# Performance work log

Measured on AMD Instinct MI355X. Metric: run time of the kernel, lower is better.

The kernel has to match this reference:

```python
import jax, jax.numpy as jnp
import numpy as np

N, E = 50000, 800000
H, C_HID = 4, 64  # heads, hidden_units
C_IN, C_OUT = 256, 64
NEG_SLOPE = 0.2
EPS = 1e-16


def gat_conv(x, src, dst, W, att_src, att_dst, bias):
    """PyG GATConv with concat=False (mean over heads) + bias.
    x: [N, F_in], W: [F_in, H*C], att_*: [H, C], bias: [C]."""
    n = x.shape[0]
    h = (x @ W).reshape(n, H, -1)                     # [N, H, C]
    a_src = jnp.sum(h * att_src, axis=-1)             # [N, H]
    a_dst = jnp.sum(h * att_dst, axis=-1)             # [N, H]
    e = jax.nn.leaky_relu(a_src[src] + a_dst[dst], NEG_SLOPE)  # [E, H]
    # segment softmax grouped by destination node
    m = jax.ops.segment_max(e, dst, num_segments=n)   # [N, H]
    e = jnp.exp(e - m[dst])
    denom = jax.ops.segment_sum(e, dst, num_segments=n)
    alpha = e / (denom[dst] + EPS)                    # [E, H]
    msg = h[src] * alpha[:, :, None]                  # [E, H, C]
    out = jax.ops.segment_sum(msg, dst, num_segments=n)  # [N, H, C]
    return out.mean(axis=1) + bias                    # concat=False -> head mean


def setup_inputs() -> dict:
    key = jax.random.key(0)
    ks = jax.random.split(key, 16)
    inp = {
        "x": jax.random.normal(ks[0], (N, C_IN), dtype=jnp.float32),
        "edge_index": jax.random.randint(ks[1], (2, E), 0, N, dtype=jnp.int64),
    }
    dims = [(C_IN, C_HID), (C_HID, C_HID), (C_HID, C_OUT)]
    for i, (fi, fo) in enumerate(dims, start=1):
        inp[f"W{i}"] = jax.random.normal(ks[2 + 4 * (i - 1)], (fi, H * fo), dtype=jnp.float32) * (1.0 / np.sqrt(fi))
        inp[f"as{i}"] = jax.random.normal(ks[3 + 4 * (i - 1)], (H, fo), dtype=jnp.float32) * 0.1
        inp[f"ad{i}"] = jax.random.normal(ks[4 + 4 * (i - 1)], (H, fo), dtype=jnp.float32) * 0.1
        inp[f"b{i}"] = jnp.zeros((fo,), dtype=jnp.float32)
    return inp


def reference(x, edge_index, W1, as1, ad1, b1, W2, as2, ad2, b2, W3, as3, ad3, b3):
    n = x.shape[0]
    loop = jnp.arange(n, dtype=edge_index.dtype)
    src = jnp.concatenate([edge_index[0], loop])  # add_self_loops=True (PyG default)
    dst = jnp.concatenate([edge_index[1], loop])
    layers = [(W1, as1, ad1, b1), (W2, as2, ad2, b2), (W3, as3, ad3, b3)]
    for (W, a_s, a_d, b) in layers:
        x = gat_conv(x, src, dst, W, a_s, a_d, b)
        x = jax.nn.relu(x)  # dropout is identity at inference
    return jax.nn.log_softmax(x, axis=-1)
```

## Files before the change

kernel.cpp:

```cpp
#include <hip/hip_runtime.h>
#include <hip/hip_bf16.h>
#include <math.h>
#include <stdint.h>

#define HEADS 4
#define CH 64
#define HC 256
#define NEG 0.2f
#define EPSV 1e-16f
#define NEGBIG -3.0e38f

typedef __attribute__((ext_vector_type(8))) short short8;
typedef __attribute__((ext_vector_type(4))) float f32x4;
typedef _Float16 f16_t;
typedef __fp16 fp16x2 __attribute__((ext_vector_type(2)));

__device__ __forceinline__ float lrelu(float x) { return x > 0.f ? x : NEG * x; }

__device__ __forceinline__ unsigned short f2bf(float f) {
  __hip_bfloat16 b = __float2bfloat16(f);
  return *reinterpret_cast<unsigned short*>(&b);
}
__device__ __forceinline__ float bf2f(unsigned short u) {
  return __uint_as_float((unsigned)u << 16);
}
__device__ __forceinline__ unsigned int pkf16(float a, float b) {
  fp16x2 v = __builtin_amdgcn_cvt_pkrtz(a, b);
  return __builtin_bit_cast(unsigned int, v);
}
__device__ __forceinline__ float dot2acc(unsigned int a, unsigned int h, float acc) {
#if __has_builtin(__builtin_amdgcn_fdot2)
  return __builtin_amdgcn_fdot2(__builtin_bit_cast(fp16x2, a),
                                __builtin_bit_cast(fp16x2, h), acc, false);
#else
  fp16x2 av = __builtin_bit_cast(fp16x2, a);
  fp16x2 hv = __builtin_bit_cast(fp16x2, h);
  return acc + (float)av[0] * (float)hv[0] + (float)av[1] * (float)hv[1];
#endif
}

__global__ __launch_bounds__(256) void wprep_k(const float* __restrict__ W,
                                               unsigned short* __restrict__ Wt,
                                               int K) {
  int i = blockIdx.x * 256 + threadIdx.x;
  if (i >= K * 256) return;
  int k = i >> 8, n = i & 255;
  Wt[(size_t)n * K + k] = f2bf(W[i]);
}

__global__ __launch_bounds__(256) void mfma_gat_k(const float* __restrict__ Af,
                                                  const unsigned short* __restrict__ Ab,
                                                  const unsigned short* __restrict__ Wt,
                                                  const float* __restrict__ att_s,
                                                  const float* __restrict__ att_d,
                                                  unsigned short* __restrict__ ht16,
                                                  float* __restrict__ a_src,
                                                  float* __restrict__ a_dst,
                                                  int M, int K, int a_is_f32) {
  __shared__ unsigned short As[32 * 40];
  __shared__ unsigned short Bs[256 * 40];
  __shared__ unsigned short Cs[32 * 258];

  int tid = threadIdx.x;
  int bm = blockIdx.x * 32;
  int w = tid >> 6, l = tid & 63;
  int lr = l & 15, lk = l >> 4;
  int row_s = tid >> 3, seg = tid & 7;

  f32x4 acc[2][4];
  #pragma unroll
  for (int rt = 0; rt < 2; ++rt)
    #pragma unroll
    for (int ct = 0; ct < 4; ++ct) {
      f32x4 z = {0.f, 0.f, 0.f, 0.f};
      acc[rt][ct] = z;
    }

  for (int k0 = 0; k0 < K; k0 += 32) {
    if (a_is_f32) {
      float4 v = make_float4(0.f, 0.f, 0.f, 0.f);
      if (bm + row_s < M)
        v = *reinterpret_cast<const float4*>(Af + (size_t)(bm + row_s) * K + k0 + seg * 4);
      ushort4 u;
      u.x = f2bf(v.x); u.y = f2bf(v.y); u.z = f2bf(v.z); u.w = f2bf(v.w);
      *reinterpret_cast<ushort4*>(&As[row_s * 40 + seg * 4]) = u;
    } else {
      ushort4 u = make_ushort4(0, 0, 0, 0);
      if (bm + row_s < M)
        u = *reinterpret_cast<const ushort4*>(Ab + (size_t)(bm + row_s) * K + k0 + seg * 4);
      *reinterpret_cast<ushort4*>(&As[row_s * 40 + seg * 4]) = u;
    }
    {
      const uint4* srcq = reinterpret_cast<const uint4*>(Wt + (size_t)tid * K + k0);
      uint4 q0 = srcq[0], q1 = srcq[1], q2 = srcq[2], q3 = srcq[3];
      uint4* dstq = reinterpret_cast<uint4*>(&Bs[tid * 40]);
      dstq[0] = q0; dstq[1] = q1; dstq[2] = q2; dstq[3] = q3;
    }
    __syncthreads();
    short8 bfr[4];
    #pragma unroll
    for (int ct = 0; ct < 4; ++ct)
      bfr[ct] = *reinterpret_cast<const short8*>(&Bs[(w * 64 + ct * 16 + lr) * 40 + lk * 8]);
    #pragma unroll
    for (int rt = 0; rt < 2; ++rt) {
      short8 af = *reinterpret_cast<const short8*>(&As[(rt * 16 + lr) * 40 + lk * 8]);
      #pragma unroll
      for (int ct = 0; ct < 4; ++ct)
        acc[rt][ct] = __builtin_amdgcn_mfma_f32_16x16x32_bf16(af, bfr[ct], acc[rt][ct], 0, 0, 0);
    }
    __syncthreads();
  }

  #pragma unroll
  for (int rt = 0; rt < 2; ++rt)
    #pragma unroll
    for (int ct = 0; ct < 4; ++ct)
      #pragma unroll
      for (int r = 0; r < 4; ++r) {
        int row = rt * 16 + lk * 4 + r;
        int c = ct * 16 + lr;
        Cs[row * 258 + c * 4 + w] = __builtin_bit_cast(unsigned short, (f16_t)acc[rt][ct][r]);
      }
  __syncthreads();

  if (bm + row_s < M) {
    ushort4* dst = reinterpret_cast<ushort4*>(ht16 + (size_t)(bm + row_s) * HC + seg * 32);
    const unsigned short* srcp = &Cs[row_s * 258 + seg * 32];
    #pragma unroll
    for (int q = 0; q < 4; ++q)
      dst[q] = *reinterpret_cast<const ushort4*>(srcp + q * 4);
  }

  {
    int nd = tid >> 3, q = tid & 7, h = q >> 1, half = q & 1;
    float ps = 0.f, pd = 0.f;
    const float* ats = att_s + h * 64 + half * 32;
    const float* atd = att_d + h * 64 + half * 32;
    const unsigned short* cp = &Cs[nd * 258 + (half * 32) * 4 + h];
    #pragma unroll
    for (int c = 0; c < 32; ++c) {
      float hv = (float)__builtin_bit_cast(f16_t, cp[c * 4]);
      ps += hv * ats[c];
      pd += hv * atd[c];
    }
    ps += __shfl_xor(ps, 1);
    pd += __shfl_xor(pd, 1);
    if (!(q & 1) && bm + nd < M) {
      a_src[(size_t)(bm + nd) * 4 + h] = ps;
      a_dst[(size_t)(bm + nd) * 4 + h] = pd;
    }
  }
}

__global__ __launch_bounds__(256) void zero2_k(int* __restrict__ a, int* __restrict__ b, int n) {
  int i = blockIdx.x * blockDim.x + threadIdx.x;
  if (i < n) { a[i] = 0; b[i] = 0; }
}

__global__ __launch_bounds__(256) void hist_k(const int* __restrict__ dst, int* __restrict__ count, int E) {
  int e = blockIdx.x * blockDim.x + threadIdx.x;
  if (e < E) atomicAdd(&count[dst[e]], 1);
}

__global__ __launch_bounds__(512) void scan1_k(const int* __restrict__ count,
                                               int* __restrict__ rp,
                                               int* __restrict__ bsum, int n) {
  __shared__ int sh[512];
  int tx = threadIdx.x;
  int i = blockIdx.x * 512 + tx;
  int v = (i < n) ? count[i] : 0;
  sh[tx] = v;
  __syncthreads();
  #pragma unroll
  for (int off = 1; off < 512; off <<= 1) {
    int t = (tx >= off) ? sh[tx - off] : 0;
    __syncthreads();
    sh[tx] += t;
    __syncthreads();
  }
  if (i < n) rp[i] = sh[tx] - v;
  if (tx == 511) bsum[blockIdx.x] = sh[511];
}

__global__ __launch_bounds__(128) void scan2_k(int* __restrict__ bsum, int nb) {
  __shared__ int sh[128];
  int tx = threadIdx.x;
  int v = (tx < nb) ? bsum[tx] : 0;
  sh[tx] = v;
  __syncthreads();
  #pragma unroll
  for (int off = 1; off < 128; off <<= 1) {
    int t = (tx >= off) ? sh[tx - off] : 0;
    __syncthreads();
    sh[tx] += t;
    __syncthreads();
  }
  if (tx < nb) bsum[tx] = sh[tx] - v;
}

__global__ __launch_bounds__(512) void scan3_k(int* __restrict__ rp, const int* __restrict__ bsum,
                                               int n, int E) {
  int i = blockIdx.x * 512 + threadIdx.x;
  if (i < n) rp[i] += bsum[blockIdx.x];
  if (i == 0) rp[n] = E;
}

__global__ __launch_bounds__(256) void scatter_k(const int* __restrict__ src, const int* __restrict__ dst,
                                                 const int* __restrict__ rp, int* __restrict__ cursor,
                                                 int* __restrict__ csr_src, int E) {
  int e = blockIdx.x * blockDim.x + threadIdx.x;
  if (e >= E) return;
  int d = dst[e];
  int pos = rp[d] + atomicAdd(&cursor[d], 1);
  csr_src[pos] = src[e];
}

__global__ __launch_bounds__(256) void soft_agg_k(const int* __restrict__ rp,
                                                  const int* __restrict__ csr_src,
                                                  const float* __restrict__ a_src,
                                                  const float* __restrict__ a_dst,
                                                  const unsigned short* __restrict__ ht16,
                                                  const float* __restrict__ bias,
                                                  float* __restrict__ outf,
                                                  unsigned short* __restrict__ outb,
                                                  int N, int do_lsm) {
  __shared__ uint4 rec[4][64];
  int tid  = threadIdx.x;
  int w    = tid >> 6;
  int lane = tid & 63;
  int wid  = (blockIdx.x * blockDim.x + tid) >> 6;
  if (wid >= N) return;
  int rs = rp[wid], re = rp[wid + 1];

  float4 ad4 = *reinterpret_cast<const float4*>(a_dst + (size_t)wid * 4);
  float4 asn = *reinterpret_cast<const float4*>(a_src + (size_t)wid * 4);
  float es0 = lrelu(asn.x + ad4.x), es1 = lrelu(asn.y + ad4.y);
  float es2 = lrelu(asn.z + ad4.z), es3 = lrelu(asn.w + ad4.w);

  int sreg = 0;
  float e0 = NEGBIG, e1 = NEGBIG, e2 = NEGBIG, e3 = NEGBIG;
  if (rs + lane < re) {
    sreg = csr_src[rs + lane];
    float4 a = *reinterpret_cast<const float4*>(a_src + (size_t)sreg * 4);
    e0 = lrelu(a.x + ad4.x); e1 = lrelu(a.y + ad4.y);
    e2 = lrelu(a.z + ad4.z); e3 = lrelu(a.w + ad4.w);
  }
  float m0 = fmaxf(es0, e0), m1 = fmaxf(es1, e1);
  float m2 = fmaxf(es2, e2), m3 = fmaxf(es3, e3);
  for (int base = rs + 64; base < re; base += 64) {
    if (base + lane < re) {
      int s = csr_src[base + lane];
      float4 a = *reinterpret_cast<const float4*>(a_src + (size_t)s * 4);
      m0 = fmaxf(m0, lrelu(a.x + ad4.x)); m1 = fmaxf(m1, lrelu(a.y + ad4.y));
      m2 = fmaxf(m2, lrelu(a.z + ad4.z)); m3 = fmaxf(m3, lrelu(a.w + ad4.w));
    }
  }
  #pragma unroll
  for (int off = 32; off > 0; off >>= 1) {
    m0 = fmaxf(m0, __shfl_xor(m0, off));
    m1 = fmaxf(m1, __shfl_xor(m1, off));
    m2 = fmaxf(m2, __shfl_xor(m2, off));
    m3 = fmaxf(m3, __shfl_xor(m3, off));
  }

  float px = expf(e0 - m0), py = expf(e1 - m1);
  float pz = expf(e2 - m2), pw = expf(e3 - m3);
  float dn0 = px, dn1 = py, dn2 = pz, dn3 = pw;
  for (int base = rs + 64; base < re; base += 64) {
    if (base + lane < re) {
      int s = csr_src[base + lane];
      float4 a = *reinterpret_cast<const float4*>(a_src + (size_t)s * 4);
      dn0 += expf(lrelu(a.x + ad4.x) - m0); dn1 += expf(lrelu(a.y + ad4.y) - m1);
      dn2 += expf(lrelu(a.z + ad4.z) - m2); dn3 += expf(lrelu(a.w + ad4.w) - m3);
    }
  }
  #pragma unroll
  for (int off = 32; off > 0; off >>= 1) {
    dn0 += __shfl_xor(dn0, off);
    dn1 += __shfl_xor(dn1, off);
    dn2 += __shfl_xor(dn2, off);
    dn3 += __shfl_xor(dn3, off);
  }
  float sp0 = expf(es0 - m0), sp1 = expf(es1 - m1);
  float sp2 = expf(es2 - m2), sp3 = expf(es3 - m3);
  dn0 += sp0; dn1 += sp1; dn2 += sp2; dn3 += sp3;
  float rr0 = 1.f / (dn0 + EPSV), rr1 = 1.f / (dn1 + EPSV);
  float rr2 = 1.f / (dn2 + EPSV), rr3 = 1.f / (dn3 + EPSV);

  float acc = 0.f;
  uint4* recw = &rec[w][0];
  const unsigned short* hl = ht16 + lane * 4;

  auto agg_lds = [&](int cnt) {
    int k = 0;
    for (; k + 4 <= cnt; k += 4) {
      uint4 r0 = recw[k + 0], r1 = recw[k + 1], r2 = recw[k + 2], r3 = recw[k + 3];
      int s0 = __builtin_amdgcn_readfirstlane((int)r0.x);
      int s1 = __builtin_amdgcn_readfirstlane((int)r1.x);
      int s2 = __builtin_amdgcn_readfirstlane((int)r2.x);
      int s3 = __builtin_amdgcn_readfirstlane((int)r3.x);
      uint2 h0 = *reinterpret_cast<const uint2*>(hl + (size_t)s0 * HC);
      uint2 h1 = *reinterpret_cast<const uint2*>(hl + (size_t)s1 * HC);
      uint2 h2 = *reinterpret_cast<const uint2*>(hl + (size_t)s2 * HC);
      uint2 h3 = *reinterpret_cast<const uint2*>(hl + (size_t)s3 * HC);
      acc = dot2acc(r0.y, h0.x, acc); acc = dot2acc(r0.z, h0.y, acc);
      acc = dot2acc(r1.y, h1.x, acc); acc = dot2acc(r1.z, h1.y, acc);
      acc = dot2acc(r2.y, h2.x, acc); acc = dot2acc(r2.z, h2.y, acc);
      acc = dot2acc(r3.y, h3.x, acc); acc = dot2acc(r3.z, h3.y, acc);
    }
    for (; k < cnt; ++k) {
      uint4 r0 = recw[k];
      int s0 = __builtin_amdgcn_readfirstlane((int)r0.x);
      uint2 hv = *reinterpret_cast<const uint2*>(hl + (size_t)s0 * HC);
      acc = dot2acc(r0.y, hv.x, acc);
      acc = dot2acc(r0.z, hv.y, acc);
    }
  };

  {
    recw[lane] = make_uint4((unsigned)sreg, pkf16(px * rr0, py * rr1),
                            pkf16(pz * rr2, pw * rr3), 0u);
    int cnt = re - rs; if (cnt > 64) cnt = 64;
    agg_lds(cnt);
  }
  for (int base = rs + 64; base < re; base += 64) {
    int s = 0;
    float f0 = NEGBIG, f1 = NEGBIG, f2 = NEGBIG, f3 = NEGBIG;
    if (base + lane < re) {
      s = csr_src[base + lane];
      float4 a = *reinterpret_cast<const float4*>(a_src + (size_t)s * 4);
      f0 = lrelu(a.x + ad4.x); f1 = lrelu(a.y + ad4.y);
      f2 = lrelu(a.z + ad4.z); f3 = lrelu(a.w + ad4.w);
    }
    float qx = expf(f0 - m0) * rr0, qy = expf(f1 - m1) * rr1;
    float qz = expf(f2 - m2) * rr2, qw = expf(f3 - m3) * rr3;
    recw[lane] = make_uint4((unsigned)s, pkf16(qx, qy), pkf16(qz, qw), 0u);
    int cnt = re - base; if (cnt > 64) cnt = 64;
    agg_lds(cnt);
  }

  uint2 shv = *reinterpret_cast<const uint2*>(ht16 + (size_t)wid * HC + lane * 4);
  acc = dot2acc(pkf16(sp0 * rr0, sp1 * rr1), shv.x, acc);
  acc = dot2acc(pkf16(sp2 * rr2, sp3 * rr3), shv.y, acc);
  float v = acc * 0.25f + bias[lane];
  v = fmaxf(v, 0.f);
  if (do_lsm) {
    float mx = v;
    #pragma unroll
    for (int off = 32; off > 0; off >>= 1) mx = fmaxf(mx, __shfl_xor(mx, off));
    float ex = expf(v - mx);
    float sm = ex;
    #pragma unroll
    for (int off = 32; off > 0; off >>= 1) sm += __shfl_xor(sm, off);
    outf[(size_t)wid * CH + lane] = v - mx - logf(sm);
  } else {
    outb[(size_t)wid * CH + lane] = f2bf(v);
  }
}

extern "C" void kernel_launch(void* const* d_in, const int* in_sizes, int n_in,
                              void* d_out, int out_size, void* d_ws, size_t ws_size,
                              hipStream_t stream) {
  const float* x0 = (const float*)d_in[0];
  const int*   ei = (const int*)d_in[1];
  int N = in_sizes[0] / HC;
  int E = in_sizes[1] / 2;
  const int* srcp = ei;
  const int* dstp = ei + E;

  const float* W[3]  = {(const float*)d_in[2], (const float*)d_in[6],  (const float*)d_in[10]};
  const float* AS[3] = {(const float*)d_in[3], (const float*)d_in[7],  (const float*)d_in[11]};
  const float* AD[3] = {(const float*)d_in[4], (const float*)d_in[8],  (const float*)d_in[12]};
  const float* BI[3] = {(const float*)d_in[5], (const float*)d_in[9],  (const float*)d_in[13]};
  int Kdim[3] = {256, 64, 64};

  char* ws = (char*)d_ws;
  size_t off = 0;
  auto alloc = [&](size_t bytes) {
    void* p = ws + off;
    off += (bytes + 255) & ~(size_t)255;
    return p;
  };
  unsigned short* ht16    = (unsigned short*)alloc((size_t)N * HC * 2);
  unsigned short* xb16    = (unsigned short*)alloc((size_t)N * CH * 2);
  float*          a_s     = (float*)alloc((size_t)N * 4 * 4);
  float*          a_d     = (float*)alloc((size_t)N * 4 * 4);
  int*            rowp    = (int*)alloc((size_t)(N + 1) * 4);
  int*            cursor  = (int*)alloc((size_t)N * 4);
  int*            csr_src = (int*)alloc((size_t)E * 4);
  int*            bsum    = (int*)alloc(512 * 4);
  unsigned short* Wt[3];
  Wt[0] = (unsigned short*)alloc((size_t)256 * 256 * 2);
  Wt[1] = (unsigned short*)alloc((size_t)256 * 64 * 2);
  Wt[2] = (unsigned short*)alloc((size_t)256 * 64 * 2);

  for (int L = 0; L < 3; ++L) {
    int tot = Kdim[L] * 256;
    wprep_k<<<(tot + 255) / 256, 256, 0, stream>>>(W[L], Wt[L], Kdim[L]);
  }

  int nb = (N + 511) / 512;
  zero2_k<<<(N + 255) / 256, 256, 0, stream>>>(cursor, rowp, N);
  hist_k<<<(E + 255) / 256, 256, 0, stream>>>(dstp, rowp, E);
  scan1_k<<<nb, 512, 0, stream>>>(rowp, rowp, bsum, N);
  scan2_k<<<1, 128, 0, stream>>>(bsum, nb);
  scan3_k<<<nb, 512, 0, stream>>>(rowp, bsum, N, E);
  scatter_k<<<(E + 255) / 256, 256, 0, stream>>>(srcp, dstp, rowp, cursor, csr_src, E);

  for (int L = 0; L < 3; ++L) {
    int K = Kdim[L];
    mfma_gat_k<<<(N + 31) / 32, 256, 0, stream>>>(
        (L == 0) ? x0 : nullptr, (L == 0) ? nullptr : xb16,
        Wt[L], AS[L], AD[L], ht16, a_s, a_d, N, K, (L == 0) ? 1 : 0);
    soft_agg_k<<<(N + 3) / 4, 256, 0, stream>>>(rowp, csr_src, a_s, a_d, ht16, BI[L],
                                                (float*)d_out, xb16, N, (L == 2) ? 1 : 0);
  }
}
```

Baseline: 391.8 us.

## Remap softmax lanes to 16 edges x 4 heads in aggregation kernel

The per-destination softmax now assigns each lane one (edge, head) pair, 16 edges by 4 heads per wavefront, instead of one edge with all four heads. Each lane computes one exp instead of four and reduces over 16 lanes rather than 64. Average degree is about 17, so this keeps more lanes busy on the score pass. The cost is more loop trips over 16-edge chunks, scalar a_src loads in place of float4 loads, and LDS records assembled from per-head half-precision writes.

New measurement: 383.9 us. 2.0% less time.

```diff
diff --git a/kernel.cpp b/kernel.cpp
--- a/kernel.cpp
+++ b/kernel.cpp
@@ -21,12 +21,8 @@
   __hip_bfloat16 b = __float2bfloat16(f);
   return *reinterpret_cast<unsigned short*>(&b);
 }
-__device__ __forceinline__ float bf2f(unsigned short u) {
-  return __uint_as_float((unsigned)u << 16);
-}
-__device__ __forceinline__ unsigned int pkf16(float a, float b) {
-  fp16x2 v = __builtin_amdgcn_cvt_pkrtz(a, b);
-  return __builtin_bit_cast(unsigned int, v);
+__device__ __forceinline__ unsigned short f16b(float f) {
+  return __builtin_bit_cast(unsigned short, (f16_t)f);
 }
 __device__ __forceinline__ float dot2acc(unsigned int a, unsigned int h, float acc) {
 #if __has_builtin(__builtin_amdgcn_fdot2)
@@ -119,7 +115,7 @@
       for (int r = 0; r < 4; ++r) {
         int row = rt * 16 + lk * 4 + r;
         int c = ct * 16 + lr;
-        Cs[row * 258 + c * 4 + w] = __builtin_bit_cast(unsigned short, (f16_t)acc[rt][ct][r]);
+        Cs[row * 258 + c * 4 + w] = f16b(acc[rt][ct][r]);
       }
   __syncthreads();
 
@@ -224,124 +220,115 @@
                                                   float* __restrict__ outf,
                                                   unsigned short* __restrict__ outb,
                                                   int N, int do_lsm) {
-  __shared__ uint4 rec[4][64];
+  __shared__ uint4 rec[4][17];
   int tid  = threadIdx.x;
   int w    = tid >> 6;
   int lane = tid & 63;
   int wid  = (blockIdx.x * blockDim.x + tid) >> 6;
   if (wid >= N) return;
   int rs = rp[wid], re = rp[wid + 1];
-
-  float4 ad4 = *reinterpret_cast<const float4*>(a_dst + (size_t)wid * 4);
-  float4 asn = *reinterpret_cast<const float4*>(a_src + (size_t)wid * 4);
-  float es0 = lrelu(asn.x + ad4.x), es1 = lrelu(asn.y + ad4.y);
-  float es2 = lrelu(asn.z + ad4.z), es3 = lrelu(asn.w + ad4.w);
-
-  int sreg = 0;
-  float e0 = NEGBIG, e1 = NEGBIG, e2 = NEGBIG, e3 = NEGBIG;
-  if (rs + lane < re) {
-    sreg = csr_src[rs + lane];
-    float4 a = *reinterpret_cast<const float4*>(a_src + (size_t)sreg * 4);
-    e0 = lrelu(a.x + ad4.x); e1 = lrelu(a.y + ad4.y);
-    e2 = lrelu(a.z + ad4.z); e3 = lrelu(a.w + ad4.w);
-  }
-  float m0 = fmaxf(es0, e0), m1 = fmaxf(es1, e1);
-  float m2 = fmaxf(es2, e2), m3 = fmaxf(es3, e3);
-  for (int base = rs + 64; base < re; base += 64) {
-    if (base + lane < re) {
-      int s = csr_src[base + lane];
-      float4 a = *reinterpret_cast<const float4*>(a_src + (size_t)s * 4);
-      m0 = fmaxf(m0, lrelu(a.x + ad4.x)); m1 = fmaxf(m1, lrelu(a.y + ad4.y));
-      m2 = fmaxf(m2, lrelu(a.z + ad4.z)); m3 = fmaxf(m3, lrelu(a.w + ad4.w));
-    }
-  }
-  #pragma unroll
-  for (int off = 32; off > 0; off >>= 1) {
-    m0 = fmaxf(m0, __shfl_xor(m0, off));
-    m1 = fmaxf(m1, __shfl_xor(m1, off));
-    m2 = fmaxf(m2, __shfl_xor(m2, off));
-    m3 = fmaxf(m3, __shfl_xor(m3, off));
-  }
-
-  float px = expf(e0 - m0), py = expf(e1 - m1);
-  float pz = expf(e2 - m2), pw = expf(e3 - m3);
-  float dn0 = px, dn1 = py, dn2 = pz, dn3 = pw;
-  for (int base = rs + 64; base < re; base += 64) {
-    if (base + lane < re) {
-      int s = csr_src[base + lane];
-      float4 a = *reinterpret_cast<const float4*>(a_src + (size_t)s * 4);
-      dn0 += expf(lrelu(a.x + ad4.x) - m0); dn1 += expf(lrelu(a.y + ad4.y) - m1);
-      dn2 += expf(lrelu(a.z + ad4.z) - m2); dn3 += expf(lrelu(a.w + ad4.w) - m3);
-    }
-  }
-  #pragma unroll
-  for (int off = 32; off > 0; off >>= 1) {
-    dn0 += __shfl_xor(dn0, off);
-    dn1 += __shfl_xor(dn1, off);
-    dn2 += __shfl_xor(dn2, off);
-    dn3 += __shfl_xor(dn3, off);
-  }
-  float sp0 = expf(es0 - m0), sp1 = expf(es1 - m1);
-  float sp2 = expf(es2 - m2), sp3 = expf(es3 - m3);
-  dn0 += sp0; dn1 += sp1; dn2 += sp2; dn3 += sp3;
-  float rr0 = 1.f / (dn0 + EPSV), rr1 = 1.f / (dn1 + EPSV);
-  float rr2 = 1.f / (dn2 + EPSV), rr3 = 1.f / (dn3 + EPSV);
-
+  int ep = lane & 15;
+  int h  = lane >> 4;
+
+  float adh = a_dst[(size_t)wid * 4 + h];
+  float ash = a_src[(size_t)wid * 4 + h];
+  float es  = lrelu(ash + adh);
+
+  int s0 = 0, s1 = 0;
+  float e0 = NEGBIG, e1 = NEGBIG;
+  if (rs + ep < re) {
+    s0 = csr_src[rs + ep];
+    e0 = lrelu(a_src[(size_t)s0 * 4 + h] + adh);
+  }
+  if (rs + 16 + ep < re) {
+    s1 = csr_src[rs + 16 + ep];
+    e1 = lrelu(a_src[(size_t)s1 * 4 + h] + adh);
+  }
+  float m = fmaxf(es, fmaxf(e0, e1));
+  for (int base = rs + 32; base < re; base += 16) {
+    if (base + ep < re) {
+      int s = csr_src[base + ep];
+      m = fmaxf(m, lrelu(a_src[(size_t)s * 4 + h] + adh));
+    }
+  }
+  #pragma unroll
+  for (int off = 8; off > 0; off >>= 1) m = fmaxf(m, __shfl_xor(m, off));
+
+  float p0 = expf(e0 - m), p1 = expf(e1 - m);
+  float dn = p0 + p1;
+  for (int base = rs + 32; base < re; base += 16) {
+    if (base + ep < re) {
+      int s = csr_src[base + ep];
+      dn += expf(lrelu(a_src[(size_t)s * 4 + h] + adh) - m);
+    }
+  }
+  #pragma unroll
+  for (int off = 8; off > 0; off >>= 1) dn += __shfl_xor(dn, off);
+  float sp = expf(es - m);
+  dn += sp;
+  float rr = 1.f / (dn + EPSV);
+
+  unsigned short* recb = reinterpret_cast<unsigned short*>(&rec[w][0]);
   float acc = 0.f;
-  uint4* recw = &rec[w][0];
   const unsigned short* hl = ht16 + lane * 4;
 
-  auto agg_lds = [&](int cnt) {
+  auto agg = [&](int cnt) {
     int k = 0;
     for (; k + 4 <= cnt; k += 4) {
-      uint4 r0 = recw[k + 0], r1 = recw[k + 1], r2 = recw[k + 2], r3 = recw[k + 3];
-      int s0 = __builtin_amdgcn_readfirstlane((int)r0.x);
-      int s1 = __builtin_amdgcn_readfirstlane((int)r1.x);
-      int s2 = __builtin_amdgcn_readfirstlane((int)r2.x);
-      int s3 = __builtin_amdgcn_readfirstlane((int)r3.x);
-      uint2 h0 = *reinterpret_cast<const uint2*>(hl + (size_t)s0 * HC);
-      uint2 h1 = *reinterpret_cast<const uint2*>(hl + (size_t)s1 * HC);
-      uint2 h2 = *reinterpret_cast<const uint2*>(hl + (size_t)s2 * HC);
-      uint2 h3 = *reinterpret_cast<const uint2*>(hl + (size_t)s3 * HC);
-      acc = dot2acc(r0.y, h0.x, acc); acc = dot2acc(r0.z, h0.y, acc);
-      acc = dot2acc(r1.y, h1.x, acc); acc = dot2acc(r1.z, h1.y, acc);
-      acc = dot2acc(r2.y, h2.x, acc); acc = dot2acc(r2.z, h2.y, acc);
-      acc = dot2acc(r3.y, h3.x, acc); acc = dot2acc(r3.z, h3.y, acc);
+      uint4 r0 = rec[w][k + 0], r1 = rec[w][k + 1];
+      uint4 r2 = rec[w][k + 2], r3 = rec[w][k + 3];
+      int t0 = __builtin_amdgcn_readfirstlane((int)r0.z);
+      int t1 = __builtin_amdgcn_readfirstlane((int)r1.z);
+      int t2 = __builtin_amdgcn_readfirstlane((int)r2.z);
+      int t3 = __builtin_amdgcn_readfirstlane((int)r3.z);
+      uint2 h0 = *reinterpret_cast<const uint2*>(hl + (size_t)t0 * HC);
+      uint2 h1 = *reinterpret_cast<const uint2*>(hl + (size_t)t1 * HC);
+      uint2 h2 = *reinterpret_cast<const uint2*>(hl + (size_t)t2 * HC);
+      uint2 h3 = *reinterpret_cast<const uint2*>(hl + (size_t)t3 * HC);
+      acc = dot2acc(r0.x, h0.x, acc); acc = dot2acc(r0.y, h0.y, acc);
+      acc = dot2acc(r1.x, h1.x, acc); acc = dot2acc(r1.y, h1.y, acc);
+      acc = dot2acc(r2.x, h2.x, acc); acc = dot2acc(r2.y, h2.y, acc);
+      acc = dot2acc(r3.x, h3.x, acc); acc = dot2acc(r3.y, h3.y, acc);
     }
     for (; k < cnt; ++k) {
-      uint4 r0 = recw[k];
-      int s0 = __builtin_amdgcn_readfirstlane((int)r0.x);
-      uint2 hv = *reinterpret_cast<const uint2*>(hl + (size_t)s0 * HC);
-      acc = dot2acc(r0.y, hv.x, acc);
-      acc = dot2acc(r0.z, hv.y, acc);
+      uint4 r0 = rec[w][k];
+      int t0 = __builtin_amdgcn_readfirstlane((int)r0.z);
+      uint2 hv = *reinterpret_cast<const uint2*>(hl + (size_t)t0 * HC);
+      acc = dot2acc(r0.x, hv.x, acc);
+      acc = dot2acc(r0.y, hv.y, acc);
     }
   };
 
+  if (ep == 0) recb[16 * 8 + h] = f16b(sp * rr);
+  recb[ep * 8 + h] = f16b(p0 * rr);
+  if (h == 0) *reinterpret_cast<int*>(recb + ep * 8 + 4) = s0;
   {
-    recw[lane] = make_uint4((unsigned)sreg, pkf16(px * rr0, py * rr1),
-                            pkf16(pz * rr2, pw * rr3), 0u);
-    int cnt = re - rs; if (cnt > 64) cnt = 64;
-    agg_lds(cnt);
-  }
-  for (int base = rs + 64; base < re; base += 64) {
+    int cnt = re - rs; if (cnt > 16) cnt = 16;
+    agg(cnt);
+  }
+  if (re > rs + 16) {
+    recb[ep * 8 + h] = f16b(p1 * rr);
+    if (h == 0) *reinterpret_cast<int*>(recb + ep * 8 + 4) = s1;
+    int cnt = re - rs - 16; if (cnt > 16) cnt = 16;
+    agg(cnt);
+  }
+  for (int base = rs + 32; base < re; base += 16) {
     int s = 0;
-    float f0 = NEGBIG, f1 = NEGBIG, f2 = NEGBIG, f3 = NEGBIG;
-    if (base + lane < re) {
-      s = csr_src[base + lane];
-      float4 a = *reinterpret_cast<const float4*>(a_src + (size_t)s * 4);
-      f0 = lrelu(a.x + ad4.x); f1 = lrelu(a.y + ad4.y);
-      f2 = lrelu(a.z + ad4.z); f3 = lrelu(a.w + ad4.w);
-    }
-    float qx = expf(f0 - m0) * rr0, qy = expf(f1 - m1) * rr1;
-    float qz = expf(f2 - m2) * rr2, qw = expf(f3 - m3) * rr3;
-    recw[lane] = make_uint4((unsigned)s, pkf16(qx, qy), pkf16(qz, qw), 0u);
-    int cnt = re - base; if (cnt > 64) cnt = 64;
-    agg_lds(cnt);
-  }
-
+    float e = NEGBIG;
+    if (base + ep < re) {
+      s = csr_src[base + ep];
+      e = lrelu(a_src[(size_t)s * 4 + h] + adh);
+    }
+    recb[ep * 8 + h] = f16b(expf(e - m) * rr);
+    if (h == 0) *reinterpret_cast<int*>(recb + ep * 8 + 4) = s;
+    int cnt = re - base; if (cnt > 16) cnt = 16;
+    agg(cnt);
+  }
+
+  uint2 sa = *reinterpret_cast<const uint2*>(&rec[w][16]);
   uint2 shv = *reinterpret_cast<const uint2*>(ht16 + (size_t)wid * HC + lane * 4);
-  acc = dot2acc(pkf16(sp0 * rr0, sp1 * rr1), shv.x, acc);
-  acc = dot2acc(pkf16(sp2 * rr2, sp3 * rr3), shv.y, acc);
+  acc = dot2acc(sa.x, shv.x, acc);
+  acc = dot2acc(sa.y, shv.y, acc);
   float v = acc * 0.25f + bias[lane];
   v = fmaxf(v, 0.f);
   if (do_lsm) {
```
